# Kernel tuning notes

Measured on AMD Instinct MI355X. Metric: run time of the kernel, lower is better.

Reference implementation:

```python
import jax, jax.numpy as jnp
import numpy as np

ALPHA = 0.2  # LeakyReLU slope
EPS = 1e-16


def _spgat_layer(x, W, a, row, col, N, concat):
    # h: [N, d]
    h = x @ W
    d = h.shape[1]
    # edge attention: a^T [h_row || h_col]  (pyGAT SpGAT: exp(-leakyrelu(.)))
    f_src = h @ a[:d]   # [N]
    f_dst = h @ a[d:]   # [N]
    e = jnp.exp(-jax.nn.leaky_relu(f_src[row] + f_dst[col], ALPHA))  # [E]
    denom = jax.ops.segment_sum(e, row, num_segments=N) + EPS        # [N]
    num = jax.ops.segment_sum(e[:, None] * h[col], row, num_segments=N)  # [N, d]
    out = num / denom[:, None]
    return jax.nn.elu(out) if concat else out


def _spgat(x, W1, a1, W2, a2, edges):
    row, col = edges[0], edges[1]
    N = x.shape[0]
    h = _spgat_layer(x, W1, a1, row, col, N, concat=True)
    h = _spgat_layer(h, W2, a2, row, col, N, concat=False)
    return jax.nn.elu(h)


def setup_inputs() -> dict:
    key = jax.random.key(0)
    ks = jax.random.split(key, 20)
    VOCAB, NFEAT = 50000, 300
    N_TW, L = 50000, 16
    UV = 50000
    E = 800000
    HID, JOINT, NCLASS = 64, 128, 2
    B = 4096

    inp = {}
    # integer structure (constants)
    inp['features_index'] = jax.random.randint(ks[0], (N_TW, L), 0, VOCAB, dtype=jnp.int32)
    inp['tw_edges'] = jax.random.randint(ks[1], (2, E), 0, N_TW, dtype=jnp.int32)
    inp['ut_edges'] = jax.random.randint(ks[2], (2, E), 0, UV, dtype=jnp.int32)
    inp['tw_graph_idx'] = jax.random.randint(ks[3], (B,), 0, N_TW, dtype=jnp.int32)
    inp['ut_graph_idx'] = jax.random.randint(ks[4], (B,), 0, UV, dtype=jnp.int32)
    # learned parameters
    inp['word_emb'] = jax.random.normal(ks[5], (VOCAB, NFEAT), jnp.float32) * 0.1
    inp['user_emb'] = jax.random.normal(ks[6], (UV, NFEAT), jnp.float32) * 0.1
    def gat_params(k, din, dh, dout):
        k1, k2, k3, k4 = jax.random.split(k, 4)
        return (jax.random.normal(k1, (din, dh), jnp.float32) * (1.0 / np.sqrt(din)),
                jax.random.normal(k2, (2 * dh,), jnp.float32) * 0.1,
                jax.random.normal(k3, (dh, dout), jnp.float32) * (1.0 / np.sqrt(dh)),
                jax.random.normal(k4, (2 * dout,), jnp.float32) * 0.1)
    inp['tw_W1'], inp['tw_a1'], inp['tw_W2'], inp['tw_a2'] = gat_params(ks[7], NFEAT, HID, JOINT)
    inp['tu_W1'], inp['tu_a1'], inp['tu_W2'], inp['tu_a2'] = gat_params(ks[8], NFEAT, HID, JOINT)
    inp['weight_W'] = jax.random.uniform(ks[9], (JOINT, JOINT), jnp.float32, -0.1, 0.1)
    inp['weight_proj'] = jax.random.uniform(ks[10], (JOINT, 1), jnp.float32, -0.1, 0.1)
    inp['out_W'] = jax.random.normal(ks[11], (NCLASS, JOINT), jnp.float32) * (1.0 / np.sqrt(JOINT))
    inp['out_b'] = jnp.zeros((NCLASS,), jnp.float32)
    return inp


def reference(word_emb, user_emb, tw_W1, tw_a1, tw_W2, tw_a2,
              tu_W1, tu_a1, tu_W2, tu_a2, weight_W, weight_proj,
              out_W, out_b, features_index, tw_edges, ut_edges,
              tw_graph_idx, ut_graph_idx):
    # tweet features: mean of word embeddings per tweet  [N_tw, nfeat]
    twt_X = word_emb[features_index].mean(axis=1)
    tw_X = _spgat(twt_X, tw_W1, tw_a1, tw_W2, tw_a2, tw_edges)   # [N_tw, joint]
    tu_X = _spgat(user_emb, tu_W1, tu_a1, tu_W2, tu_a2, ut_edges)  # [uV, joint]
    # attention-weighted fusion of the two views
    u_tw = jnp.tanh(tw_X @ weight_W)
    u_tu = jnp.tanh(tu_X @ weight_W)
    att_tw = jnp.mean(u_tw @ weight_proj, axis=0)  # [1]
    att_tu = jnp.mean(u_tu @ weight_proj, axis=0)  # [1]
    att = jax.nn.softmax(jnp.concatenate([att_tw, att_tu], axis=0))  # [2]
    feat = att[0] * tw_X[tw_graph_idx] + att[1] * tu_X[ut_graph_idx]  # [B, joint]
    logits = feat @ out_W.T + out_b
    return jax.nn.log_softmax(logits, axis=1)
```

## Files before the change

kernel.cpp:

```cpp
#include <hip/hip_runtime.h>
#include <hip/hip_bf16.h>

typedef __hip_bfloat16 bf16;
typedef unsigned int uint32;
typedef __attribute__((ext_vector_type(8))) short s8v;
typedef __attribute__((ext_vector_type(4))) short s4v;
typedef __attribute__((ext_vector_type(8))) short bf8v;
typedef __attribute__((ext_vector_type(4))) float f4v;

#define CAP 64
#define CAPSH 6

__device__ __forceinline__ float waveReduce(float v) {
#pragma unroll
    for (int o = 32; o > 0; o >>= 1) v += __shfl_xor(v, o, 64);
    return v;
}

__device__ __forceinline__ short f2bf(float x) {
    __hip_bfloat16 h = __float2bfloat16(x);
    return *reinterpret_cast<short*>(&h);
}
__device__ __forceinline__ float bf2f(short s) {
    return __uint_as_float(((uint32)(unsigned short)s) << 16);
}
__device__ __forceinline__ uint32 pack2(float x, float y) {
    return (uint32)(unsigned short)f2bf(x) | (((uint32)(unsigned short)f2bf(y)) << 16);
}
__device__ __forceinline__ float blo(uint32 d) { return __uint_as_float(d << 16); }
__device__ __forceinline__ float bhi(uint32 d) { return __uint_as_float(d & 0xffff0000u); }
__device__ __forceinline__ float felu(float x) { return x > 0.f ? x : __expf(x) - 1.f; }

struct WJobs {
    const float* src[5];
    short* dst[5];
    int K[5], N[5], KP[5], total[5];
    int* cursor;
    float* attsum;
    int N2;
};
__global__ void wtrans_all(WJobs jb) {
    int j = blockIdx.y;
    int i = blockIdx.x * blockDim.x + threadIdx.x;
    if (j == 5) {
        if (i < jb.N2) jb.cursor[i] = i << CAPSH;
        if (i < 2) jb.attsum[i] = 0.f;
        return;
    }
    if (i >= jb.total[j]) return;
    int KP = jb.KP[j];
    int n = i / KP, k = i - n * KP;
    jb.dst[j][i] = f2bf(k < jb.K[j] ? jb.src[j][(size_t)k * jb.N[j] + n] : 0.f);
}

struct GJob {
    const void* A;
    const short* Wt;
    const float* av;
    void* C;
    float* fs;
    float* fd;
    int M;
};

template <typename AT, int K, int KPAD, int N, int CSTORE, bool DO_F, bool DO_ATT>
__global__ __launch_bounds__(256) void mfma_gemm(GJob j0, GJob j1, int nb0,
                                                 float* __restrict__ attsum, int bnd) {
    constexpr int NT = N / 16;
    constexpr int NP = KPAD / 64;
    __shared__ short As[64 * 72];
    __shared__ short Ws[N * 72];
    __shared__ float red[8];
    int t = threadIdx.x;
    int lane = t & 63;
    int wid = t >> 6;
    int col = lane & 15;
    int quad = lane >> 4;

    int bid = blockIdx.x;
    bool sec = bid >= nb0;
    GJob J = sec ? j1 : j0;
    const AT* A = (const AT*)J.A;
    const short* Wt = J.Wt;
    const float* av = J.av;
    int M = J.M;
    int row0 = (sec ? bid - nb0 : bid) * 64;

    f4v acc[NT];
#pragma unroll
    for (int i = 0; i < NT; ++i) { f4v z = {0.f, 0.f, 0.f, 0.f}; acc[i] = z; }

    for (int p = 0; p < NP; ++p) {
        int k0 = p * 64;
        if constexpr (sizeof(AT) == 4) {
            const float4* A4 = (const float4*)A;
            int f = t & 15, r0 = t >> 4;
#pragma unroll
            for (int r = r0; r < 64; r += 16) {
                int gr = row0 + r;
                int f4i = (k0 >> 2) + f;
                float4 v = {0.f, 0.f, 0.f, 0.f};
                if (gr < M && f4i < K / 4) v = A4[(size_t)gr * (K / 4) + f4i];
                s4v sv = {f2bf(v.x), f2bf(v.y), f2bf(v.z), f2bf(v.w)};
                *(s4v*)&As[r * 72 + f * 4] = sv;
            }
        } else {
            int c8 = t & 7, r0 = t >> 3;
#pragma unroll
            for (int r = r0; r < 64; r += 32) {
                int gr = row0 + r;
                s8v v = {0, 0, 0, 0, 0, 0, 0, 0};
                if (gr < M) v = *(const s8v*)&A[(size_t)gr * K + k0 + c8 * 8];
                *(s8v*)&As[r * 72 + c8 * 8] = v;
            }
        }
        {
            int c8 = t & 7, r0 = t >> 3;
#pragma unroll
            for (int r = r0; r < N; r += 32)
                *(s8v*)&Ws[r * 72 + c8 * 8] = *(const s8v*)&Wt[(size_t)r * KPAD + k0 + c8 * 8];
        }
        __syncthreads();
#pragma unroll
        for (int c2 = 0; c2 < 2; ++c2) {
            int ko = c2 * 32 + quad * 8;
            bf8v af = *(const bf8v*)&As[(wid * 16 + col) * 72 + ko];
#pragma unroll
            for (int nt = 0; nt < NT; ++nt) {
                bf8v bf = *(const bf8v*)&Ws[(nt * 16 + col) * 72 + ko];
                acc[nt] = __builtin_amdgcn_mfma_f32_16x16x32_bf16(af, bf, acc[nt], 0, 0, 0);
            }
        }
        __syncthreads();
    }

    int mbase = row0 + wid * 16;
    if constexpr (CSTORE == 1) {
        float* C = (float*)J.C;
#pragma unroll
        for (int nt = 0; nt < NT; ++nt)
#pragma unroll
            for (int r = 0; r < 4; ++r) {
                int gr = mbase + quad * 4 + r;
                if (gr < M) C[(size_t)gr * N + nt * 16 + col] = acc[nt][r];
            }
    } else if constexpr (CSTORE == 2) {
        short* C = (short*)J.C;
#pragma unroll
        for (int nt = 0; nt < NT; ++nt)
#pragma unroll
            for (int r = 0; r < 4; ++r) {
                int gr = mbase + quad * 4 + r;
                if (gr < M) C[(size_t)gr * N + nt * 16 + col] = f2bf(acc[nt][r]);
            }
    }
    if constexpr (DO_F) {
        if (av) {
            float* fs = J.fs;
            float* fd = J.fd;
            float a0[NT], a1[NT];
#pragma unroll
            for (int nt = 0; nt < NT; ++nt) {
                a0[nt] = av[nt * 16 + col];
                a1[nt] = av[N + nt * 16 + col];
            }
#pragma unroll
            for (int r = 0; r < 4; ++r) {
                float p0 = 0.f, p1 = 0.f;
#pragma unroll
                for (int nt = 0; nt < NT; ++nt) {
                    p0 += acc[nt][r] * a0[nt];
                    p1 += acc[nt][r] * a1[nt];
                }
#pragma unroll
                for (int o = 8; o > 0; o >>= 1) {
                    p0 += __shfl_xor(p0, o, 64);
                    p1 += __shfl_xor(p1, o, 64);
                }
                int gr = mbase + quad * 4 + r;
                if (col == 0 && gr < M) { fs[gr] = p0; fd[gr] = p1; }
            }
        }
    }
    if constexpr (DO_ATT) {
        float s0 = 0.f, s1 = 0.f;
#pragma unroll
        for (int nt = 0; nt < NT; ++nt) {
            float pj = av[nt * 16 + col];
#pragma unroll
            for (int r = 0; r < 4; ++r) {
                int gr = mbase + quad * 4 + r;
                float v = tanhf(acc[nt][r]) * pj;
                if (gr < bnd) s0 += v; else s1 += v;
            }
        }
        s0 = waveReduce(s0);
        s1 = waveReduce(s1);
        if (lane == 0) { red[wid] = s0; red[4 + wid] = s1; }
        __syncthreads();
        if (t == 0) {
            atomicAdd(attsum + 0, red[0] + red[1] + red[2] + red[3]);
            atomicAdd(attsum + 1, red[4] + red[5] + red[6] + red[7]);
        }
    }
}

__global__ void gather_h64(const int* __restrict__ idx, const uint32* __restrict__ P,
                           const float* __restrict__ a,
                           short* __restrict__ H, float* __restrict__ fsv, float* __restrict__ fdv,
                           int N) {
    int wv = (blockIdx.x * blockDim.x + threadIdx.x) >> 6;
    int lane = threadIdx.x & 63;
    if (wv >= N) return;
    int hf = lane >> 5, li = lane & 31;
    const int* ip = idx + wv * 16;
    float a0 = 0.f, a1 = 0.f;
#pragma unroll
    for (int t = 0; t < 8; ++t) {
        int ind = ip[2 * t + hf];
        uint32 d = P[(size_t)ind * 32 + li];
        a0 += blo(d);
        a1 += bhi(d);
    }
    a0 += __shfl_xor(a0, 32, 64);
    a1 += __shfl_xor(a1, 32, 64);
    a0 *= 0.0625f;
    a1 *= 0.0625f;
    if (hf == 0) ((uint32*)H)[(size_t)wv * 32 + li] = pack2(a0, a1);
    float cp = hf ? 0.f : (a0 * a[2 * li] + a1 * a[2 * li + 1]);
    float cq = hf ? 0.f : (a0 * a[64 + 2 * li] + a1 * a[64 + 2 * li + 1]);
    float p = waveReduce(cp);
    float q = waveReduce(cq);
    if (lane == 0) { fsv[wv] = p; fdv[wv] = q; }
}

__global__ void scatter_win_kernel(const int* __restrict__ rowA, const int* __restrict__ colA,
                                   const int* __restrict__ rowB, const int* __restrict__ colB,
                                   int* __restrict__ cursor, int* __restrict__ ecol,
                                   int E, int N, int w0, int w1) {
    int i = blockIdx.x * blockDim.x + threadIdx.x;
    if (i < E) {
        int r = rowA[i];
        if (r >= w0 && r < w1) {
            int p = atomicAdd(&cursor[r], 1);
            if (p < (r << CAPSH) + CAP) ecol[p] = colA[i];
        }
    } else if (i < 2 * E) {
        int r = N + rowB[i - E];
        if (r >= w0 && r < w1) {
            int p = atomicAdd(&cursor[r], 1);
            if (p < (r << CAPSH) + CAP) ecol[p] = colB[i - E];
        }
    }
}

__global__ void agg64f_kernel(const int* __restrict__ cursor, const int* __restrict__ ecol,
                              const float* __restrict__ fs, const float* __restrict__ fd,
                              const uint32* __restrict__ hb, uint32* __restrict__ out,
                              int N2, int NTW) {
    int wv = (blockIdx.x * blockDim.x + threadIdx.x) >> 6;
    int lane = threadIdx.x & 63;
    if (wv >= N2) return;
    int s = wv << CAPSH;
    int ne = min(cursor[wv] - s, CAP);
    int coff = wv < NTW ? 0 : NTW;
    float fsr = fs[wv];
    int cl = 0;
    float el = 0.f;
    if (lane < ne) {
        cl = ecol[s + lane];
        float f = fsr + fd[coff + cl];
        el = __expf(-(f >= 0.f ? f : 0.2f * f));
    }
    int qd = lane >> 4, li = lane & 15;
    const uint2* h2 = (const uint2*)hb;
    float a0 = 0.f, a1 = 0.f, a2 = 0.f, a3 = 0.f, den = 0.f;
    for (int kb = 0; kb < ne; kb += 16) {
        int k0 = kb + qd, k1 = kb + 4 + qd, k2 = kb + 8 + qd, k3 = kb + 12 + qd;
        int c0 = __shfl(cl, k0, 64); float e0 = __shfl(el, k0, 64);
        int c1 = __shfl(cl, k1, 64); float e1 = __shfl(el, k1, 64);
        int c2 = __shfl(cl, k2, 64); float e2 = __shfl(el, k2, 64);
        int c3 = __shfl(cl, k3, 64); float e3 = __shfl(el, k3, 64);
        uint2 d0 = h2[(size_t)(coff + c0) * 16 + li];
        uint2 d1 = h2[(size_t)(coff + c1) * 16 + li];
        uint2 d2 = h2[(size_t)(coff + c2) * 16 + li];
        uint2 d3 = h2[(size_t)(coff + c3) * 16 + li];
        a0 += e0 * blo(d0.x) + e1 * blo(d1.x) + e2 * blo(d2.x) + e3 * blo(d3.x);
        a1 += e0 * bhi(d0.x) + e1 * bhi(d1.x) + e2 * bhi(d2.x) + e3 * bhi(d3.x);
        a2 += e0 * blo(d0.y) + e1 * blo(d1.y) + e2 * blo(d2.y) + e3 * blo(d3.y);
        a3 += e0 * bhi(d0.y) + e1 * bhi(d1.y) + e2 * bhi(d2.y) + e3 * bhi(d3.y);
        den += e0 + e1 + e2 + e3;
    }
    a0 += __shfl_xor(a0, 16, 64); a0 += __shfl_xor(a0, 32, 64);
    a1 += __shfl_xor(a1, 16, 64); a1 += __shfl_xor(a1, 32, 64);
    a2 += __shfl_xor(a2, 16, 64); a2 += __shfl_xor(a2, 32, 64);
    a3 += __shfl_xor(a3, 16, 64); a3 += __shfl_xor(a3, 32, 64);
    den += __shfl_xor(den, 16, 64); den += __shfl_xor(den, 32, 64);
    if (lane < 16) {
        float inv = 1.f / (den + 1e-16f);
        float v0 = felu(a0 * inv);
        float v1 = felu(a1 * inv);
        float v2 = felu(a2 * inv);
        float v3 = felu(a3 * inv);
        uint2 o = {pack2(v0, v1), pack2(v2, v3)};
        ((uint2*)out)[(size_t)wv * 16 + li] = o;
    }
}

__global__ void agg128f_kernel(const int* __restrict__ cursor, const int* __restrict__ ecol,
                               const float* __restrict__ fs, const float* __restrict__ fd,
                               const uint32* __restrict__ hb, uint32* __restrict__ out,
                               int N2, int NTW) {
    int wv = (blockIdx.x * blockDim.x + threadIdx.x) >> 6;
    int lane = threadIdx.x & 63;
    if (wv >= N2) return;
    int s = wv << CAPSH;
    int ne = min(cursor[wv] - s, CAP);
    int coff = wv < NTW ? 0 : NTW;
    float fsr = fs[wv];
    int cl = 0;
    float el = 0.f;
    if (lane < ne) {
        cl = ecol[s + lane];
        float f = fsr + fd[coff + cl];
        el = __expf(-(f >= 0.f ? f : 0.2f * f));
    }
    int hf = lane >> 5, li = lane & 31;
    const uint2* h2 = (const uint2*)hb;
    float a0 = 0.f, a1 = 0.f, a2 = 0.f, a3 = 0.f, den = 0.f;
    for (int kb = 0; kb < ne; kb += 8) {
        int k0 = kb + hf, k1 = kb + 2 + hf, k2 = kb + 4 + hf, k3 = kb + 6 + hf;
        int c0 = __shfl(cl, k0, 64); float e0 = __shfl(el, k0, 64);
        int c1 = __shfl(cl, k1, 64); float e1 = __shfl(el, k1, 64);
        int c2 = __shfl(cl, k2, 64); float e2 = __shfl(el, k2, 64);
        int c3 = __shfl(cl, k3, 64); float e3 = __shfl(el, k3, 64);
        uint2 d0 = h2[(size_t)(coff + c0) * 32 + li];
        uint2 d1 = h2[(size_t)(coff + c1) * 32 + li];
        uint2 d2 = h2[(size_t)(coff + c2) * 32 + li];
        uint2 d3 = h2[(size_t)(coff + c3) * 32 + li];
        a0 += e0 * blo(d0.x) + e1 * blo(d1.x) + e2 * blo(d2.x) + e3 * blo(d3.x);
        a1 += e0 * bhi(d0.x) + e1 * bhi(d1.x) + e2 * bhi(d2.x) + e3 * bhi(d3.x);
        a2 += e0 * blo(d0.y) + e1 * blo(d1.y) + e2 * blo(d2.y) + e3 * blo(d3.y);
        a3 += e0 * bhi(d0.y) + e1 * bhi(d1.y) + e2 * bhi(d2.y) + e3 * bhi(d3.y);
        den += e0 + e1 + e2 + e3;
    }
    a0 += __shfl_xor(a0, 32, 64);
    a1 += __shfl_xor(a1, 32, 64);
    a2 += __shfl_xor(a2, 32, 64);
    a3 += __shfl_xor(a3, 32, 64);
    den += __shfl_xor(den, 32, 64);
    if (hf == 0) {
        float inv = 1.f / (den + 1e-16f);
        float v0 = felu(a0 * inv);
        float v1 = felu(a1 * inv);
        float v2 = felu(a2 * inv);
        float v3 = felu(a3 * inv);
        uint2 o = {pack2(v0, v1), pack2(v2, v3)};
        ((uint2*)out)[(size_t)wv * 32 + li] = o;
    }
}

__global__ void final_kernel(const short* __restrict__ twX, const short* __restrict__ tuX,
                             const int* __restrict__ twi, const int* __restrict__ tui,
                             const float* __restrict__ attsum,
                             const float* __restrict__ outW, const float* __restrict__ outb,
                             float* __restrict__ out, int B, float invNtw, float invNuv) {
    int wave = (blockIdx.x * blockDim.x + threadIdx.x) >> 6;
    int lane = threadIdx.x & 63;
    if (wave >= B) return;
    float z0 = attsum[0] * invNtw, z1 = attsum[1] * invNuv;
    float m = fmaxf(z0, z1);
    float e0 = expf(z0 - m), e1 = expf(z1 - m);
    float a0 = e0 / (e0 + e1), a1 = e1 / (e0 + e1);
    int ti = twi[wave], ui = tui[wave];
    float l0 = 0.f, l1 = 0.f;
#pragma unroll
    for (int p = 0; p < 2; ++p) {
        int j = lane + 64 * p;
        float feat = a0 * bf2f(twX[(size_t)ti * 128 + j]) + a1 * bf2f(tuX[(size_t)ui * 128 + j]);
        l0 += feat * outW[j];
        l1 += feat * outW[128 + j];
    }
    l0 = waveReduce(l0);
    l1 = waveReduce(l1);
    if (lane == 0) {
        l0 += outb[0];
        l1 += outb[1];
        float mm = fmaxf(l0, l1);
        float lse = mm + logf(expf(l0 - mm) + expf(l1 - mm));
        out[wave * 2 + 0] = l0 - lse;
        out[wave * 2 + 1] = l1 - lse;
    }
}

extern "C" void kernel_launch(void* const* d_in, const int* in_sizes, int n_in,
                              void* d_out, int out_size, void* d_ws, size_t ws_size,
                              hipStream_t stream) {
    const int* features_index = (const int*)d_in[0];
    const int* tw_edges = (const int*)d_in[1];
    const int* ut_edges = (const int*)d_in[2];
    const int* tw_gidx = (const int*)d_in[3];
    const int* ut_gidx = (const int*)d_in[4];
    const float* word_emb = (const float*)d_in[5];
    const float* user_emb = (const float*)d_in[6];
    const float* tw_W1 = (const float*)d_in[7];
    const float* tw_a1 = (const float*)d_in[8];
    const float* tw_W2 = (const float*)d_in[9];
    const float* tw_a2 = (const float*)d_in[10];
    const float* tu_W1 = (const float*)d_in[11];
    const float* tu_a1 = (const float*)d_in[12];
    const float* tu_W2 = (const float*)d_in[13];
    const float* tu_a2 = (const float*)d_in[14];
    const float* weight_W = (const float*)d_in[15];
    const float* weight_proj = (const float*)d_in[16];
    const float* out_W = (const float*)d_in[17];
    const float* out_b = (const float*)d_in[18];

    const int E = in_sizes[1] / 2;
    const int NTW = in_sizes[0] / 16;
    const int VOCAB = in_sizes[5] / 300;
    const int UV = in_sizes[6] / 300;
    const int B = in_sizes[3];
    const int N2 = NTW + UV;

    char* ws = (char*)d_ws;
    size_t off = 0;
    auto carve = [&](size_t bytes) -> void* {
        void* p = ws + off;
        off += (bytes + 255) & ~(size_t)255;
        return p;
    };
    float* Pbuf = (float*)carve((size_t)VOCAB * 64 * sizeof(float));
    short* Hb1 = (short*)carve((size_t)N2 * 64 * sizeof(short));
    short* H2 = (short*)carve((size_t)N2 * 128 * sizeof(short));
    short* X = (short*)carve((size_t)N2 * 128 * sizeof(short));
    float* f_s = (float*)carve((size_t)N2 * sizeof(float));
    float* f_d = (float*)carve((size_t)N2 * sizeof(float));
    float* attsum = (float*)carve(256);
    int* cursor = (int*)carve((size_t)N2 * sizeof(int));
    int* ecol = (int*)carve((size_t)N2 * CAP * sizeof(int));
    short* Wt1tw = (short*)carve((size_t)64 * 320 * sizeof(short));
    short* Wt1tu = (short*)carve((size_t)64 * 320 * sizeof(short));
    short* Wt2tw = (short*)carve((size_t)128 * 64 * sizeof(short));
    short* Wt2tu = (short*)carve((size_t)128 * 64 * sizeof(short));
    short* Wta   = (short*)carve((size_t)128 * 128 * sizeof(short));
    short* num1 = ((size_t)VOCAB * 64 * sizeof(float) >= (size_t)N2 * 64 * sizeof(short))
                      ? (short*)Pbuf
                      : (short*)carve((size_t)N2 * 64 * sizeof(short));
    (void)ws_size; (void)n_in; (void)out_size;

    WJobs jb;
    jb.src[0] = tw_W1;    jb.dst[0] = Wt1tw; jb.K[0] = 300; jb.N[0] = 64;  jb.KP[0] = 320; jb.total[0] = 64 * 320;
    jb.src[1] = tu_W1;    jb.dst[1] = Wt1tu; jb.K[1] = 300; jb.N[1] = 64;  jb.KP[1] = 320; jb.total[1] = 64 * 320;
    jb.src[2] = tw_W2;    jb.dst[2] = Wt2tw; jb.K[2] = 64;  jb.N[2] = 128; jb.KP[2] = 64;  jb.total[2] = 128 * 64;
    jb.src[3] = tu_W2;    jb.dst[3] = Wt2tu; jb.K[3] = 64;  jb.N[3] = 128; jb.KP[3] = 64;  jb.total[3] = 128 * 64;
    jb.src[4] = weight_W; jb.dst[4] = Wta;   jb.K[4] = 128; jb.N[4] = 128; jb.KP[4] = 128; jb.total[4] = 128 * 128;
    jb.cursor = cursor;
    jb.attsum = attsum;
    jb.N2 = N2;
    {
        int gx = (64 * 320 + 255) / 256;
        int gc = (N2 + 255) / 256;
        if (gc > gx) gx = gc;
        dim3 g(gx, 6);
        wtrans_all<<<g, 256, 0, stream>>>(jb);
    }

    int g2E = (2 * E + 255) / 256;
    {
        const int NPASS = 8;
        int W = (N2 + NPASS - 1) / NPASS;
        for (int p = 0; p < NPASS; ++p) {
            int w0 = p * W;
            int w1 = w0 + W; if (w1 > N2) w1 = N2;
            scatter_win_kernel<<<g2E, 256, 0, stream>>>(tw_edges, tw_edges + E,
                                                        ut_edges, ut_edges + E,
                                                        cursor, ecol, E, NTW, w0, w1);
        }
    }

    {
        GJob a{word_emb, Wt1tw, nullptr, Pbuf, nullptr, nullptr, VOCAB};
        GJob b{user_emb, Wt1tu, tu_a1, Hb1 + (size_t)NTW * 64, f_s + NTW, f_d + NTW, UV};
        int nbw = (VOCAB + 63) / 64, nbu = (UV + 63) / 64;
        mfma_gemm<float, 300, 320, 64, 2, true, false><<<nbw + nbu, 256, 0, stream>>>(
            a, b, nbw, nullptr, 0);
    }
    gather_h64<<<(NTW + 3) / 4, 256, 0, stream>>>(features_index, (const uint32*)Pbuf, tw_a1,
                                                  Hb1, f_s, f_d, NTW);

    agg64f_kernel<<<(N2 + 3) / 4, 256, 0, stream>>>(cursor, ecol, f_s, f_d,
                                                    (const uint32*)Hb1, (uint32*)num1, N2, NTW);

    {
        int nbtw = (NTW + 63) / 64, nbtu = (UV + 63) / 64;
        GJob a{num1, Wt2tw, tw_a2, H2, f_s, f_d, NTW};
        GJob b{num1 + (size_t)NTW * 64, Wt2tu, tu_a2, H2 + (size_t)NTW * 128,
               f_s + NTW, f_d + NTW, UV};
        mfma_gemm<short, 64, 64, 128, 2, true, false><<<nbtw + nbtu, 256, 0, stream>>>(
            a, b, nbtw, nullptr, 0);
    }

    agg128f_kernel<<<(N2 + 3) / 4, 256, 0, stream>>>(cursor, ecol, f_s, f_d,
                                                     (const uint32*)H2, (uint32*)X, N2, NTW);

    {
        GJob a{X, Wta, weight_proj, nullptr, nullptr, nullptr, N2};
        int nb = (N2 + 63) / 64;
        mfma_gemm<short, 128, 128, 128, 0, false, true><<<nb, 256, 0, stream>>>(
            a, a, nb, attsum, NTW);
    }

    final_kernel<<<(B + 3) / 4, 256, 0, stream>>>(X, X + (size_t)NTW * 128, tw_gidx, ut_gidx,
                                                  attsum, out_W, out_b, (float*)d_out, B,
                                                  1.0f / (float)NTW, 1.0f / (float)UV);
}
```

Before: 486.2 us.

## Fuse edge scatter into first GEMM launch and register-prefetch GEMM tiles

The edge-bucketing scatter moves from eight windowed passes into extra blocks of the first MFMA GEMM launch, so the atomic scatter overlaps with the embedding GEMM and seven kernel launches plus repeated edge reads go away. The GEMM main loop now loads the next K-slice into registers while the current slice is multiplied, which hides global load latency. The cost is higher register pressure. Dropping the windowing also lets atomics from all rows run at once, which may change atomic contention and ecol write locality.

After: 486.3 us. About the same (+0.0%).

```diff
diff --git a/kernel.cpp b/kernel.cpp
--- a/kernel.cpp
+++ b/kernel.cpp
@@ -62,16 +62,39 @@
     float* fd;
     int M;
 };
-
-template <typename AT, int K, int KPAD, int N, int CSTORE, bool DO_F, bool DO_ATT>
+struct SJob {
+    const int* rowA; const int* colA;
+    const int* rowB; const int* colB;
+    int* cursor; int* ecol;
+    int E; int NTW; int nbg;
+};
+
+template <typename AT, int K, int KPAD, int N, int CSTORE, bool DO_F, bool DO_ATT, bool DO_SCAT>
 __global__ __launch_bounds__(256) void mfma_gemm(GJob j0, GJob j1, int nb0,
-                                                 float* __restrict__ attsum, int bnd) {
+                                                 float* __restrict__ attsum, int bnd, SJob sj) {
     constexpr int NT = N / 16;
     constexpr int NP = KPAD / 64;
+    int t = threadIdx.x;
+
+    if constexpr (DO_SCAT) {
+        if ((int)blockIdx.x >= sj.nbg) {
+            int i = ((int)blockIdx.x - sj.nbg) * 256 + t;
+            if (i < sj.E) {
+                int r = sj.rowA[i];
+                int p0 = atomicAdd(&sj.cursor[r], 1);
+                if (p0 < (r << CAPSH) + CAP) sj.ecol[p0] = sj.colA[i];
+            } else if (i < 2 * sj.E) {
+                int r = sj.NTW + sj.rowB[i - sj.E];
+                int p0 = atomicAdd(&sj.cursor[r], 1);
+                if (p0 < (r << CAPSH) + CAP) sj.ecol[p0] = sj.colB[i - sj.E];
+            }
+            return;
+        }
+    }
+
     __shared__ short As[64 * 72];
     __shared__ short Ws[N * 72];
     __shared__ float red[8];
-    int t = threadIdx.x;
     int lane = t & 63;
     int wid = t >> 6;
     int col = lane & 15;
@@ -90,37 +113,65 @@
 #pragma unroll
     for (int i = 0; i < NT; ++i) { f4v z = {0.f, 0.f, 0.f, 0.f}; acc[i] = z; }
 
-    for (int p = 0; p < NP; ++p) {
+    float4 ra[4];
+    s8v rsa[2];
+    s8v rb[NT / 2];
+
+    auto issue = [&](int p) {
         int k0 = p * 64;
         if constexpr (sizeof(AT) == 4) {
             const float4* A4 = (const float4*)A;
             int f = t & 15, r0 = t >> 4;
 #pragma unroll
-            for (int r = r0; r < 64; r += 16) {
-                int gr = row0 + r;
+            for (int r = 0; r < 4; ++r) {
+                int gr = row0 + r0 + 16 * r;
                 int f4i = (k0 >> 2) + f;
                 float4 v = {0.f, 0.f, 0.f, 0.f};
                 if (gr < M && f4i < K / 4) v = A4[(size_t)gr * (K / 4) + f4i];
-                s4v sv = {f2bf(v.x), f2bf(v.y), f2bf(v.z), f2bf(v.w)};
-                *(s4v*)&As[r * 72 + f * 4] = sv;
+                ra[r] = v;
             }
         } else {
             int c8 = t & 7, r0 = t >> 3;
 #pragma unroll
-            for (int r = r0; r < 64; r += 32) {
-                int gr = row0 + r;
+            for (int r = 0; r < 2; ++r) {
+                int gr = row0 + r0 + 32 * r;
                 s8v v = {0, 0, 0, 0, 0, 0, 0, 0};
                 if (gr < M) v = *(const s8v*)&A[(size_t)gr * K + k0 + c8 * 8];
-                *(s8v*)&As[r * 72 + c8 * 8] = v;
+                rsa[r] = v;
             }
         }
         {
             int c8 = t & 7, r0 = t >> 3;
 #pragma unroll
-            for (int r = r0; r < N; r += 32)
-                *(s8v*)&Ws[r * 72 + c8 * 8] = *(const s8v*)&Wt[(size_t)r * KPAD + k0 + c8 * 8];
-        }
+            for (int r = 0; r < NT / 2; ++r)
+                rb[r] = *(const s8v*)&Wt[(size_t)(r0 + 32 * r) * KPAD + k0 + c8 * 8];
+        }
+    };
+    auto commit = [&]() {
+        if constexpr (sizeof(AT) == 4) {
+            int f = t & 15, r0 = t >> 4;
+#pragma unroll
+            for (int r = 0; r < 4; ++r) {
+                float4 v = ra[r];
+                s4v sv = {f2bf(v.x), f2bf(v.y), f2bf(v.z), f2bf(v.w)};
+                *(s4v*)&As[(r0 + 16 * r) * 72 + f * 4] = sv;
+            }
+        } else {
+            int c8 = t & 7, r0 = t >> 3;
+#pragma unroll
+            for (int r = 0; r < 2; ++r) *(s8v*)&As[(r0 + 32 * r) * 72 + c8 * 8] = rsa[r];
+        }
+        int c8 = t & 7, r0 = t >> 3;
+#pragma unroll
+        for (int r = 0; r < NT / 2; ++r) *(s8v*)&Ws[(r0 + 32 * r) * 72 + c8 * 8] = rb[r];
+    };
+
+    issue(0);
+    for (int p = 0; p < NP; ++p) {
         __syncthreads();
+        commit();
+        __syncthreads();
+        if (p + 1 < NP) issue(p + 1);
 #pragma unroll
         for (int c2 = 0; c2 < 2; ++c2) {
             int ko = c2 * 32 + quad * 8;
@@ -131,7 +182,6 @@
                 acc[nt] = __builtin_amdgcn_mfma_f32_16x16x32_bf16(af, bf, acc[nt], 0, 0, 0);
             }
         }
-        __syncthreads();
     }
 
     int mbase = row0 + wid * 16;
@@ -232,26 +282,6 @@
     float p = waveReduce(cp);
     float q = waveReduce(cq);
     if (lane == 0) { fsv[wv] = p; fdv[wv] = q; }
-}
-
-__global__ void scatter_win_kernel(const int* __restrict__ rowA, const int* __restrict__ colA,
-                                   const int* __restrict__ rowB, const int* __restrict__ colB,
-                                   int* __restrict__ cursor, int* __restrict__ ecol,
-                                   int E, int N, int w0, int w1) {
-    int i = blockIdx.x * blockDim.x + threadIdx.x;
-    if (i < E) {
-        int r = rowA[i];
-        if (r >= w0 && r < w1) {
-            int p = atomicAdd(&cursor[r], 1);
-            if (p < (r << CAPSH) + CAP) ecol[p] = colA[i];
-        }
-    } else if (i < 2 * E) {
-        int r = N + rowB[i - E];
-        if (r >= w0 && r < w1) {
-            int p = atomicAdd(&cursor[r], 1);
-            if (p < (r << CAPSH) + CAP) ecol[p] = colB[i - E];
-        }
-    }
 }
 
 __global__ void agg64f_kernel(const int* __restrict__ cursor, const int* __restrict__ ecol,
@@ -466,25 +496,17 @@
         wtrans_all<<<g, 256, 0, stream>>>(jb);
     }
 
-    int g2E = (2 * E + 255) / 256;
-    {
-        const int NPASS = 8;
-        int W = (N2 + NPASS - 1) / NPASS;
-        for (int p = 0; p < NPASS; ++p) {
-            int w0 = p * W;
-            int w1 = w0 + W; if (w1 > N2) w1 = N2;
-            scatter_win_kernel<<<g2E, 256, 0, stream>>>(tw_edges, tw_edges + E,
-                                                        ut_edges, ut_edges + E,
-                                                        cursor, ecol, E, NTW, w0, w1);
-        }
-    }
+    SJob sempty{nullptr, nullptr, nullptr, nullptr, nullptr, nullptr, 0, 0, 0};
 
     {
         GJob a{word_emb, Wt1tw, nullptr, Pbuf, nullptr, nullptr, VOCAB};
         GJob b{user_emb, Wt1tu, tu_a1, Hb1 + (size_t)NTW * 64, f_s + NTW, f_d + NTW, UV};
         int nbw = (VOCAB + 63) / 64, nbu = (UV + 63) / 64;
-        mfma_gemm<float, 300, 320, 64, 2, true, false><<<nbw + nbu, 256, 0, stream>>>(
-            a, b, nbw, nullptr, 0);
+        int nbg = nbw + nbu;
+        int nsc = (2 * E + 255) / 256;
+        SJob sj{tw_edges, tw_edges + E, ut_edges, ut_edges + E, cursor, ecol, E, NTW, nbg};
+        mfma_gemm<float, 300, 320, 64, 2, true, false, true><<<nbg + nsc, 256, 0, stream>>>(
+            a, b, nbw, nullptr, 0, sj);
     }
     gather_h64<<<(NTW + 3) / 4, 256, 0, stream>>>(features_index, (const uint32*)Pbuf, tw_a1,
                                                   Hb1, f_s, f_d, NTW);
@@ -497,8 +519,8 @@
         GJob a{num1, Wt2tw, tw_a2, H2, f_s, f_d, NTW};
         GJob b{num1 + (size_t)NTW * 64, Wt2tu, tu_a2, H2 + (size_t)NTW * 128,
                f_s + NTW, f_d + NTW, UV};
-        mfma_gemm<short, 64, 64, 128, 2, true, false><<<nbtw + nbtu, 256, 0, stream>>>(
-            a, b, nbtw, nullptr, 0);
+        mfma_gemm<short, 64, 64, 128, 2, true, false, false><<<nbtw + nbtu, 256, 0, stream>>>(
+            a, b, nbtw, nullptr, 0, sempty);
     }
 
     agg128f_kernel<<<(N2 + 3) / 4, 256, 0, stream>>>(cursor, ecol, f_s, f_d,
@@ -507,8 +529,8 @@
     {
         GJob a{X, Wta, weight_proj, nullptr, nullptr, nullptr, N2};
         int nb = (N2 + 63) / 64;
-        mfma_gemm<short, 128, 128, 128, 0, false, true><<<nb, 256, 0, stream>>>(
-            a, a, nb, attsum, NTW);
+        mfma_gemm<short, 128, 128, 128, 0, false, true, false><<<nb, 256, 0, stream>>>(
+            a, a, nb, attsum, NTW, sempty);
     }
 
     final_kernel<<<(B + 3) / 4, 256, 0, stream>>>(X, X + (size_t)NTW * 128, tw_gidx, ut_gidx,
```
